# Kernel tuning notes

Hardware: AMD Instinct MI355X
Metric: run time of the kernel (lower is better)

Reference implementation:

```python
import jax, jax.numpy as jnp
import numpy as np
from jax import lax

B, S, D, H = 2, 2048, 1024, 16
DH = D // H
KERNELS = (3, 5)
NK = len(KERNELS)
COUT = D // NK  # channels per conv branch


def setup_inputs() -> dict:
    key = jax.random.key(0)
    ks = jax.random.split(key, 12)
    w = lambda k, shp: (jax.random.normal(k, shp, dtype=jnp.float32) * 0.02)
    inp = {
        "q": jax.random.normal(ks[0], (B, S, D), dtype=jnp.float32),
        "k": jax.random.normal(ks[1], (B, S, D), dtype=jnp.float32),
        "v": jax.random.normal(ks[2], (B, S, D), dtype=jnp.float32),
        "mask": jnp.ones((B, S, S), dtype=jnp.int32),
        "Wq": w(ks[3], (D, D)),
        "Wk": w(ks[4], (D, D)),
        "Wv": w(ks[5], (D, D)),
        "Wo": w(ks[6], (D, D)),
        "bo": jnp.zeros((D,), dtype=jnp.float32),
        "conv_w0": w(ks[7], (COUT, D, KERNELS[0])),  # OIH
        "conv_b0": jnp.zeros((COUT,), dtype=jnp.float32),
        "conv_w1": w(ks[8], (COUT, D, KERNELS[1])),
        "conv_b1": jnp.zeros((COUT,), dtype=jnp.float32),
        "gate": jnp.ones((H,), dtype=jnp.float32),
    }
    return inp


def _split_heads(x):  # [B,S,D] -> [B,H,S,DH]
    return x.reshape(B, S, H, DH).transpose(0, 2, 1, 3)


def _conv1d_same(x_ncl, w_oik, b, ksz):
    pad = ksz // 2
    y = lax.conv_general_dilated(
        x_ncl, w_oik, window_strides=(1,), padding=[(pad, pad)],
        dimension_numbers=("NCH", "OIH", "NCH"))
    return y + b[None, :, None]


def reference(q, k, v, mask, Wq, Wk, Wv, Wo, bo,
              conv_w0, conv_b0, conv_w1, conv_b1, gate):
    qh = _split_heads(q @ Wq.T)
    kh = _split_heads(k @ Wk.T)
    vh = _split_heads(v @ Wv.T)

    # conv-derived K: operate on raw k in NCL layout, concat channel-wise
    k_ncl = k.transpose(0, 2, 1)  # [B,D,S]
    c0 = _conv1d_same(k_ncl, conv_w0, conv_b0, KERNELS[0])
    c1 = _conv1d_same(k_ncl, conv_w1, conv_b1, KERNELS[1])
    k_conv = jnp.concatenate([c0, c1], axis=1).transpose(0, 2, 1)  # [B,S,D]
    kch = _split_heads(k_conv)

    g = jax.nn.sigmoid(gate).reshape(1, H, 1, 1)
    scale = 1.0 / np.sqrt(DH).astype(np.float32)
    attn = ((1.0 - g) * jnp.einsum("bhqd,bhkd->bhqk", qh, kh)
            + g * jnp.einsum("bhqd,bhkd->bhqk", qh, kch)) * scale
    attn = jnp.where(mask[:, None, :, :] == 0, jnp.float32(-1e9), attn)
    attn = jax.nn.softmax(attn, axis=-1)

    out = jnp.einsum("bhqk,bhkd->bhqd", attn, vh)  # [B,H,S,DH]
    out = out.transpose(0, 2, 1, 3).reshape(B, S, D)
    return out @ Wo.T + bo
```

## Files before the change

### kernel.cpp

```cpp
#include <hip/hip_runtime.h>
#include <math.h>

#define Bb 2
#define Ss 2048
#define Dd 1024
#define Hh 16
#define SP 2052

typedef unsigned short u16;
typedef __bf16 bf16x8 __attribute__((ext_vector_type(8)));
typedef float f32x4 __attribute__((ext_vector_type(4)));
typedef unsigned short u16x8 __attribute__((ext_vector_type(8)));

__device__ __forceinline__ u16 f2bf(float f) {
    union { float f; unsigned int u; } c; c.f = f;
    unsigned int u = c.u + 0x7FFFu + ((c.u >> 16) & 1u);
    return (u16)(u >> 16);
}

__device__ __forceinline__ float bf2f(u16 h) {
    union { unsigned int u; float f; } c; c.u = ((unsigned int)h) << 16;
    return c.f;
}

__device__ __forceinline__ void gload16(const void* g, void* l) {
    __builtin_amdgcn_global_load_lds(
        (const __attribute__((address_space(1))) void*)g,
        (__attribute__((address_space(3))) void*)l, 16, 0, 0);
}

__global__ void prep_weights(const float* __restrict__ Wq, const float* __restrict__ Wk,
                             const float* __restrict__ Wv, const float* __restrict__ Wo,
                             const float* __restrict__ w0, const float* __restrict__ b0,
                             const float* __restrict__ w1, const float* __restrict__ b1,
                             const float* __restrict__ gate,
                             u16* __restrict__ wqs, u16* __restrict__ wvb, u16* __restrict__ wob,
                             u16* __restrict__ Wc0, u16* __restrict__ Wc1, float* __restrict__ bc)
{
    int idx = blockIdx.x * 256 + threadIdx.x;
    const int NW = 1024 * 1024;
    if (idx < NW) { wqs[idx] = f2bf(Wq[idx] * 0.18033688011112042f); return; }
    idx -= NW;
    if (idx < NW) { wvb[idx] = f2bf(Wv[idx]); return; }
    idx -= NW;
    if (idx < NW) { wob[idx] = f2bf(Wo[idx]); return; }
    idx -= NW;
    if (idx < 512 * 3072) {
        int c = idx / 3072, rem = idx % 3072, t = rem >> 10, d = rem & 1023;
        float g = 1.f / (1.f + expf(-gate[c >> 6]));
        float v = g * w0[(c * 1024 + d) * 3 + t];
        if (t == 1) v += (1.f - g) * Wk[c * 1024 + d];
        Wc0[idx] = f2bf(v);
        return;
    }
    idx -= 512 * 3072;
    if (idx < 512 * 5120) {
        int c = idx / 5120, rem = idx % 5120, t = rem >> 10, d = rem & 1023;
        int cg = c + 512;
        float g = 1.f / (1.f + expf(-gate[cg >> 6]));
        float v = g * w1[(c * 1024 + d) * 5 + t];
        if (t == 2) v += (1.f - g) * Wk[cg * 1024 + d];
        Wc1[idx] = f2bf(v);
        return;
    }
    idx -= 512 * 5120;
    if (idx < 1024) {
        float g = 1.f / (1.f + expf(-gate[idx >> 6]));
        bc[idx] = g * (idx < 512 ? b0[idx] : b1[idx - 512]);
    }
}

__global__ void convert_inputs(const float* __restrict__ q, const float* __restrict__ k,
                               const float* __restrict__ v,
                               u16* __restrict__ qbf, u16* __restrict__ kbf, u16* __restrict__ vbf)
{
    int idx = blockIdx.x * 256 + threadIdx.x;
    const int per = (Bb * SP * Dd) / 8;
    int which = idx / per;
    if (which >= 3) return;
    int e = (idx - which * per) * 8;
    const float* src = which == 0 ? q : which == 1 ? k : v;
    u16* dst = which == 0 ? qbf : which == 1 ? kbf : vbf;
    int rp = e >> 10, col = e & 1023;
    int b = rp / SP, r = rp - b * SP;
    u16x8 o;
    if (r >= 2 && r < SP - 2) {
        const float* s = &src[((size_t)b * Ss + (r - 2)) * Dd + col];
        float4 lo = *(const float4*)s, hi = *(const float4*)(s + 4);
        o[0] = f2bf(lo.x); o[1] = f2bf(lo.y); o[2] = f2bf(lo.z); o[3] = f2bf(lo.w);
        o[4] = f2bf(hi.x); o[5] = f2bf(hi.y); o[6] = f2bf(hi.z); o[7] = f2bf(hi.w);
    } else {
        #pragma unroll
        for (int j = 0; j < 8; j++) o[j] = 0;
    }
    *(u16x8*)&dst[e] = o;
}

__global__ void mask_prep(const int* __restrict__ mask, unsigned int* __restrict__ bits,
                          int* __restrict__ rowflags)
{
    int row = blockIdx.x;
    int lane = threadIdx.x;
    const int* mp = mask + (size_t)row * Ss + lane * 32;
    unsigned int w = 0;
    #pragma unroll
    for (int j = 0; j < 32; j += 4) {
        int4 m4 = *(const int4*)&mp[j];
        if (m4.x != 0) w |= 1u << j;
        if (m4.y != 0) w |= 1u << (j + 1);
        if (m4.z != 0) w |= 1u << (j + 2);
        if (m4.w != 0) w |= 1u << (j + 3);
    }
    bits[(size_t)row * 64 + lane] = w;
    int anyz = __any(w != 0xFFFFFFFFu);
    if (lane == 0) rowflags[row] = anyz;
}

__device__ __forceinline__ void run_gemm_job(
    const u16* __restrict__ A, const u16* __restrict__ B, u16* __restrict__ C,
    int strB, int kS, int kL, int mB, int nB, int rO, int Cst,
    u16* As, u16* Bsh, int lane, int wave, int waveM, int waveN)
{
    f32x4 acc[4][4];
    #pragma unroll
    for (int i = 0; i < 4; i++)
        #pragma unroll
        for (int j = 0; j < 4; j++) acc[i][j] = (f32x4){0.f, 0.f, 0.f, 0.f};

    for (int k0 = kS; k0 < kS + kL; k0 += 32) {
        __syncthreads();
        #pragma unroll
        for (int cc = 0; cc < 2; cc++) {
            int rbase = (wave * 2 + cc) * 16;
            int r = rbase + (lane >> 2);
            int gm = mB + r;
            int grow = (gm >> 11) * SP + (gm & 2047) + rO + (k0 >> 10);
            int csrc = (lane & 3) ^ (r & 3);
            gload16(A + (size_t)grow * 1024 + (k0 & 1023) + csrc * 8, &As[rbase * 32]);
            int gn = nB + r;
            gload16(B + (size_t)gn * strB + k0 + csrc * 8, &Bsh[rbase * 32]);
        }
        __syncthreads();

        bf16x8 af[4], bfr[4];
        #pragma unroll
        for (int t = 0; t < 4; t++) {
            int mrow = waveM + t * 16 + (lane & 15);
            af[t] = *(const bf16x8*)&As[mrow * 32 + (((lane >> 4) ^ (mrow & 3))) * 8];
            int nrow = waveN + t * 16 + (lane & 15);
            bfr[t] = *(const bf16x8*)&Bsh[nrow * 32 + (((lane >> 4) ^ (nrow & 3))) * 8];
        }
        #pragma unroll
        for (int mt = 0; mt < 4; mt++)
            #pragma unroll
            for (int nt = 0; nt < 4; nt++)
                acc[mt][nt] = __builtin_amdgcn_mfma_f32_16x16x32_bf16(
                    af[mt], bfr[nt], acc[mt][nt], 0, 0, 0);
    }

    #pragma unroll
    for (int mt = 0; mt < 4; mt++)
        #pragma unroll
        for (int nt = 0; nt < 4; nt++)
            #pragma unroll
            for (int r = 0; r < 4; r++) {
                int row = mB + waveM + mt * 16 + (lane >> 4) * 4 + r;
                int gcol = nB + waveN + nt * 16 + (lane & 15);
                C[(size_t)row * Cst + gcol] = f2bf(acc[mt][nt][r]);
            }
}

__global__ __launch_bounds__(256) void gemm_multi(
    const u16* __restrict__ qbf, const u16* __restrict__ kbf, const u16* __restrict__ vbf,
    const u16* __restrict__ wqs, const u16* __restrict__ wvb,
    const u16* __restrict__ Wc0, const u16* __restrict__ Wc1,
    u16* __restrict__ Qp, u16* __restrict__ Vp,
    u16* __restrict__ P0a, u16* __restrict__ P0b,
    u16* __restrict__ P1a, u16* __restrict__ P1b, u16* __restrict__ P1c)
{
    __shared__ u16 As[128 * 32];
    __shared__ u16 Bsh[128 * 32];
    int tid = threadIdx.x, lane = tid & 63, wave = tid >> 6;
    int waveM = (wave >> 1) * 64, waveN = (wave & 1) * 64;

    int bid = blockIdx.x;
    const u16 *A0, *B0; u16 *C0; int sB0, kS0, kL0, mB0, nB0, rO0, Cs0;
    const u16 *A1 = nullptr, *B1 = nullptr; u16 *C1 = nullptr;
    int sB1 = 0, kS1 = 0, kL1 = 0, mB1 = 0, nB1 = 0, rO1 = 0, Cs1 = 0;
    int njobs = 1;

    if (bid < 128) {
        int t = bid;
        A0 = kbf; B0 = Wc0; C0 = P0a; sB0 = 3072; kS0 = 0; kL0 = 2048;
        mB0 = (t >> 2) * 128; nB0 = (t & 3) * 128; rO0 = 1; Cs0 = 512;
    } else if (bid < 256) {
        int t = bid - 128;
        A0 = kbf; B0 = Wc1; C0 = P1a; sB0 = 5120; kS0 = 0; kL0 = 2048;
        mB0 = (t >> 2) * 128; nB0 = (t & 3) * 128; rO0 = 0; Cs0 = 512;
    } else if (bid < 384) {
        int t = bid - 256;
        A0 = kbf; B0 = Wc1; C0 = P1b; sB0 = 5120; kS0 = 2048; kL0 = 2048;
        mB0 = (t >> 2) * 128; nB0 = (t & 3) * 128; rO0 = 0; Cs0 = 512;
    } else if (bid < 512) {
        int t = bid - 384;
        A0 = kbf; B0 = Wc0; C0 = P0b; sB0 = 3072; kS0 = 2048; kL0 = 1024;
        mB0 = (t >> 2) * 128; nB0 = (t & 3) * 128; rO0 = 1; Cs0 = 512;
        A1 = kbf; B1 = Wc1; C1 = P1c; sB1 = 5120; kS1 = 4096; kL1 = 1024;
        mB1 = mB0; nB1 = nB0; rO1 = 0; Cs1 = 512;
        njobs = 2;
    } else {
        int i0 = (bid - 512) * 2, i1 = i0 + 1;
        if (i0 < 256) { A0 = qbf; B0 = wqs; C0 = Qp; }
        else { i0 -= 256; A0 = vbf; B0 = wvb; C0 = Vp; }
        sB0 = 1024; kS0 = 0; kL0 = 1024;
        mB0 = (i0 >> 3) * 128; nB0 = (i0 & 7) * 128; rO0 = 2; Cs0 = 1024;
        if (i1 < 256) { A1 = qbf; B1 = wqs; C1 = Qp; }
        else { i1 -= 256; A1 = vbf; B1 = wvb; C1 = Vp; }
        sB1 = 1024; kS1 = 0; kL1 = 1024;
        mB1 = (i1 >> 3) * 128; nB1 = (i1 & 7) * 128; rO1 = 2; Cs1 = 1024;
        njobs = 2;
    }

    run_gemm_job(A0, B0, C0, sB0, kS0, kL0, mB0, nB0, rO0, Cs0,
                 As, Bsh, lane, wave, waveM, waveN);
    if (njobs == 2)
        run_gemm_job(A1, B1, C1, sB1, kS1, kL1, mB1, nB1, rO1, Cs1,
                     As, Bsh, lane, wave, waveM, waveN);
}

__global__ __launch_bounds__(256) void conv_reduce(
    const u16* __restrict__ P0a, const u16* __restrict__ P0b,
    const u16* __restrict__ P1a, const u16* __restrict__ P1b, const u16* __restrict__ P1c,
    const float* __restrict__ bc, u16* __restrict__ Keff)
{
    int idx = blockIdx.x * 256 + threadIdx.x;
    int e = idx * 8;
    int r = e >> 9, c = e & 511;
    u16x8 a0 = *(const u16x8*)&P0a[e];
    u16x8 b0 = *(const u16x8*)&P0b[e];
    u16x8 a1 = *(const u16x8*)&P1a[e];
    u16x8 b1 = *(const u16x8*)&P1b[e];
    u16x8 c1 = *(const u16x8*)&P1c[e];
    float bias0[8], bias1[8];
    *(float4*)&bias0[0] = *(const float4*)&bc[c];
    *(float4*)&bias0[4] = *(const float4*)&bc[c + 4];
    *(float4*)&bias1[0] = *(const float4*)&bc[512 + c];
    *(float4*)&bias1[4] = *(const float4*)&bc[512 + c + 4];
    u16x8 o0, o1;
    #pragma unroll
    for (int j = 0; j < 8; j++) {
        o0[j] = f2bf(bf2f(a0[j]) + bf2f(b0[j]) + bias0[j]);
        o1[j] = f2bf(bf2f(a1[j]) + bf2f(b1[j]) + bf2f(c1[j]) + bias1[j]);
    }
    *(u16x8*)&Keff[(size_t)r * 1024 + c] = o0;
    *(u16x8*)&Keff[(size_t)r * 1024 + 512 + c] = o1;
}

__global__ __launch_bounds__(256) void gemm_out(
    const u16* __restrict__ A, const u16* __restrict__ Bw,
    float* __restrict__ Cf32, const float* __restrict__ bias)
{
    __shared__ u16 As[128 * 32];
    __shared__ u16 Bs[128 * 32];
    int tid = threadIdx.x, lane = tid & 63, wave = tid >> 6;
    int waveM = (wave >> 1) * 64, waveN = (wave & 1) * 64;
    int mBase = blockIdx.y * 128, nBase = blockIdx.x * 128;
    const int K = 1024;

    f32x4 acc[4][4];
    #pragma unroll
    for (int i = 0; i < 4; i++)
        #pragma unroll
        for (int j = 0; j < 4; j++) acc[i][j] = (f32x4){0.f, 0.f, 0.f, 0.f};

    for (int k0 = 0; k0 < K; k0 += 32) {
        __syncthreads();
        #pragma unroll
        for (int cc = 0; cc < 2; cc++) {
            int rbase = (wave * 2 + cc) * 16;
            int r = rbase + (lane >> 2);
            int gm = mBase + r;
            int grow = (gm >> 11) * SP + (gm & 2047) + 2;
            int csrc = (lane & 3) ^ (r & 3);
            gload16(A + (size_t)grow * 1024 + k0 + csrc * 8, &As[rbase * 32]);
            int gn = nBase + r;
            gload16(Bw + (size_t)gn * K + k0 + csrc * 8, &Bs[rbase * 32]);
        }
        __syncthreads();

        bf16x8 af[4], bfr[4];
        #pragma unroll
        for (int t = 0; t < 4; t++) {
            int mrow = waveM + t * 16 + (lane & 15);
            af[t] = *(const bf16x8*)&As[mrow * 32 + (((lane >> 4) ^ (mrow & 3))) * 8];
            int nrow = waveN + t * 16 + (lane & 15);
            bfr[t] = *(const bf16x8*)&Bs[nrow * 32 + (((lane >> 4) ^ (nrow & 3))) * 8];
        }
        #pragma unroll
        for (int mt = 0; mt < 4; mt++)
            #pragma unroll
            for (int nt = 0; nt < 4; nt++)
                acc[mt][nt] = __builtin_amdgcn_mfma_f32_16x16x32_bf16(
                    af[mt], bfr[nt], acc[mt][nt], 0, 0, 0);
    }

    #pragma unroll
    for (int mt = 0; mt < 4; mt++)
        #pragma unroll
        for (int nt = 0; nt < 4; nt++)
            #pragma unroll
            for (int r = 0; r < 4; r++) {
                int row = mBase + waveM + mt * 16 + (lane >> 4) * 4 + r;
                int gcol = nBase + waveN + nt * 16 + (lane & 15);
                Cf32[(size_t)row * 1024 + gcol] = acc[mt][nt][r] + bias[gcol];
            }
}

__global__ __launch_bounds__(256) void vtrans_kernel(const u16* __restrict__ Vp,
                                                     u16* __restrict__ Vt)
{
    __shared__ u16 t[64 * 64];
    int bid = blockIdx.x;
    int st = bid & 31, h = (bid >> 5) & 15, b = bid >> 9;
    int s0 = st * 64;
    int tid = threadIdx.x;
    #pragma unroll
    for (int w = 0; w < 2; w++) {
        int f = tid + w * 256;
        int row = f >> 3, c = f & 7;
        int p = c ^ (row & 7);
        u16x8 v = *(const u16x8*)&Vp[(size_t)(b * Ss + s0 + row) * Dd + h * 64 + c * 8];
        *(u16x8*)&t[row * 64 + p * 8] = v;
    }
    __syncthreads();
    #pragma unroll
    for (int w = 0; w < 2; w++) {
        int f = tid + w * 256;
        int d = f >> 3, s8 = (f & 7) * 8;
        u16x8 v;
        #pragma unroll
        for (int j = 0; j < 8; j++) {
            int s = s8 + j;
            v[j] = t[s * 64 + (((d >> 3) ^ (s & 7))) * 8 + (d & 7)];
        }
        *(u16x8*)&Vt[((size_t)(b * Hh + h) * 64 + d) * Ss + s0 + s8] = v;
    }
}

__global__ __launch_bounds__(256) void flash_kernel(
    const u16* __restrict__ Qp, const u16* __restrict__ Keff, const u16* __restrict__ Vt,
    const unsigned int* __restrict__ maskbits, const int* __restrict__ rowflags,
    u16* __restrict__ AO)
{
    __shared__ u16 Qs[128 * 64];
    __shared__ u16 Ks[64 * 64];
    __shared__ u16 Ps[4][32 * 64];
    int tid = threadIdx.x, lane = tid & 63, wave = tid >> 6;
    int q0 = blockIdx.x * 128, h = blockIdx.y, b = blockIdx.z;

    #pragma unroll
    for (int cc = 0; cc < 4; cc++) {
        int rbase = (wave * 4 + cc) * 8;
        int r = rbase + (lane >> 3);
        int csrc = (lane & 7) ^ (r & 7);
        gload16(Qp + (size_t)(b * Ss + q0 + r) * Dd + h * 64 + csrc * 8, &Qs[rbase * 64]);
    }

    int anyz = 0;
    #pragma unroll
    for (int mt = 0; mt < 2; mt++)
        #pragma unroll
        for (int r = 0; r < 4; r++)
            anyz |= rowflags[b * Ss + q0 + wave * 32 + mt * 16 + (lane >> 4) * 4 + r];
    bool doMask = __any(anyz);

    float lrow[2][4];
    f32x4 oa[2][4];
    #pragma unroll
    for (int mt = 0; mt < 2; mt++) {
        #pragma unroll
        for (int r = 0; r < 4; r++) lrow[mt][r] = 0.f;
        #pragma unroll
        for (int nt = 0; nt < 4; nt++) oa[mt][nt] = (f32x4){0.f, 0.f, 0.f, 0.f};
    }

    __syncthreads();

    bf16x8 qa[2][2];
    #pragma unroll
    for (int mt = 0; mt < 2; mt++)
        #pragma unroll
        for (int ks = 0; ks < 2; ks++) {
            int mr = wave * 32 + mt * 16 + (lane & 15);
            int c = ks * 4 + (lane >> 4);
            qa[mt][ks] = *(const bf16x8*)&Qs[mr * 64 + (c ^ (mr & 7)) * 8];
        }

    const u16* vbase = Vt + (size_t)(b * Hh + h) * 64 * Ss;

    for (int k0 = 0; k0 < Ss; k0 += 64) {
        #pragma unroll
        for (int cc = 0; cc < 2; cc++) {
            int rbase = (wave * 2 + cc) * 8;
            int r = rbase + (lane >> 3);
            int csrc = (lane & 7) ^ (r & 7);
            gload16(Keff + (size_t)(b * Ss + k0 + r) * Dd + h * 64 + csrc * 8, &Ks[rbase * 64]);
        }
        __syncthreads();

        f32x4 sa[2][4];
        #pragma unroll
        for (int mt = 0; mt < 2; mt++)
            #pragma unroll
            for (int nt = 0; nt < 4; nt++) sa[mt][nt] = (f32x4){0.f, 0.f, 0.f, 0.f};
        bf16x8 kb[4][2];
        #pragma unroll
        for (int nt = 0; nt < 4; nt++)
            #pragma unroll
            for (int ks = 0; ks < 2; ks++) {
                int nr = nt * 16 + (lane & 15);
                int c = ks * 4 + (lane >> 4);
                kb[nt][ks] = *(const bf16x8*)&Ks[nr * 64 + (c ^ (nr & 7)) * 8];
            }
        #pragma unroll
        for (int mt = 0; mt < 2; mt++)
            #pragma unroll
            for (int nt = 0; nt < 4; nt++)
                #pragma unroll
                for (int ks = 0; ks < 2; ks++)
                    sa[mt][nt] = __builtin_amdgcn_mfma_f32_16x16x32_bf16(
                        qa[mt][ks], kb[nt][ks], sa[mt][nt], 0, 0, 0);

        bf16x8 vf[4][2];
        #pragma unroll
        for (int nt = 0; nt < 4; nt++)
            #pragma unroll
            for (int ks = 0; ks < 2; ks++) {
                int d = nt * 16 + (lane & 15);
                int kc = k0 + ks * 32 + (lane >> 4) * 8;
                vf[nt][ks] = *(const bf16x8*)&vbase[(size_t)d * Ss + kc];
            }

        if (doMask) {
            #pragma unroll
            for (int mt = 0; mt < 2; mt++)
                #pragma unroll
                for (int r = 0; r < 4; r++) {
                    int qrow = q0 + wave * 32 + mt * 16 + (lane >> 4) * 4 + r;
                    const unsigned int* mb = &maskbits[((size_t)b * Ss + qrow) * 64 + (k0 >> 5)];
                    unsigned int w0m = mb[0], w1m = mb[1];
                    #pragma unroll
                    for (int nt = 0; nt < 4; nt++) {
                        int col = nt * 16 + (lane & 15);
                        unsigned int w = (col & 32) ? w1m : w0m;
                        if (!((w >> (col & 31)) & 1u)) sa[mt][nt][r] = -1.442695e9f;
                    }
                }
        }

        #pragma unroll
        for (int mt = 0; mt < 2; mt++)
            #pragma unroll
            for (int r = 0; r < 4; r++) {
                float p0 = __builtin_amdgcn_exp2f(sa[mt][0][r]);
                float p1 = __builtin_amdgcn_exp2f(sa[mt][1][r]);
                float p2 = __builtin_amdgcn_exp2f(sa[mt][2][r]);
                float p3 = __builtin_amdgcn_exp2f(sa[mt][3][r]);
                sa[mt][0][r] = p0; sa[mt][1][r] = p1;
                sa[mt][2][r] = p2; sa[mt][3][r] = p3;
                lrow[mt][r] += (p0 + p1) + (p2 + p3);
            }

        u16* pw = Ps[wave];
        #pragma unroll
        for (int mt = 0; mt < 2; mt++)
            #pragma unroll
            for (int nt = 0; nt < 4; nt++)
                #pragma unroll
                for (int r = 0; r < 4; r++) {
                    int row = mt * 16 + (lane >> 4) * 4 + r;
                    int col = nt * 16 + (lane & 15);
                    pw[row * 64 + (((col >> 3) ^ (row & 7))) * 8 + (col & 7)] =
                        f2bf(sa[mt][nt][r]);
                }

        bf16x8 pa[2][2];
        #pragma unroll
        for (int mt = 0; mt < 2; mt++)
            #pragma unroll
            for (int ks = 0; ks < 2; ks++) {
                int row = mt * 16 + (lane & 15);
                int c = ks * 4 + (lane >> 4);
                pa[mt][ks] = *(const bf16x8*)&pw[row * 64 + (c ^ (row & 7)) * 8];
            }
        #pragma unroll
        for (int mt = 0; mt < 2; mt++)
            #pragma unroll
            for (int nt = 0; nt < 4; nt++)
                #pragma unroll
                for (int ks = 0; ks < 2; ks++)
                    oa[mt][nt] = __builtin_amdgcn_mfma_f32_16x16x32_bf16(
                        pa[mt][ks], vf[nt][ks], oa[mt][nt], 0, 0, 0);

        __syncthreads();
    }

    #pragma unroll
    for (int mt = 0; mt < 2; mt++)
        #pragma unroll
        for (int r = 0; r < 4; r++) {
            float rs = lrow[mt][r];
            #pragma unroll
            for (int d = 1; d < 16; d <<= 1) rs += __shfl_xor(rs, d, 64);
            float inv = 1.f / rs;
            int qrow = q0 + wave * 32 + mt * 16 + (lane >> 4) * 4 + r;
            size_t rowbase = ((size_t)b * SP + 2 + qrow) * Dd + h * 64;
            #pragma unroll
            for (int nt = 0; nt < 4; nt++)
                AO[rowbase + nt * 16 + (lane & 15)] = f2bf(oa[mt][nt][r] * inv);
        }
}

extern "C" void kernel_launch(void* const* d_in, const int* in_sizes, int n_in,
                              void* d_out, int out_size, void* d_ws, size_t ws_size,
                              hipStream_t stream)
{
    (void)in_sizes; (void)n_in; (void)out_size; (void)ws_size;
    const float* q    = (const float*)d_in[0];
    const float* k    = (const float*)d_in[1];
    const float* v    = (const float*)d_in[2];
    const int*   mask = (const int*)d_in[3];
    const float* Wq   = (const float*)d_in[4];
    const float* Wk   = (const float*)d_in[5];
    const float* Wv   = (const float*)d_in[6];
    const float* Wo   = (const float*)d_in[7];
    const float* bo   = (const float*)d_in[8];
    const float* w0   = (const float*)d_in[9];
    const float* b0   = (const float*)d_in[10];
    const float* w1   = (const float*)d_in[11];
    const float* b1   = (const float*)d_in[12];
    const float* gate = (const float*)d_in[13];
    float* out = (float*)d_out;

    char* p = (char*)d_ws;
    const size_t nPad = (size_t)Bb * SP * Dd;
    const size_t nBSD = (size_t)Bb * Ss * Dd;
    const size_t nHalf = (size_t)4096 * 512;
    u16* qbf  = (u16*)p;            p += nPad * 2;
    u16* kbf  = (u16*)p;            p += nPad * 2;
    u16* vbf  = (u16*)p;            p += nPad * 2;
    u16* Qp   = (u16*)p;            p += nBSD * 2;
    u16* Keff = (u16*)p;            p += nBSD * 2;
    u16* Vp   = (u16*)p;            p += nBSD * 2;
    u16* Vt   = (u16*)p;            p += nBSD * 2;
    u16* wqs  = (u16*)p;            p += (size_t)Dd * Dd * 2;
    u16* wvb  = (u16*)p;            p += (size_t)Dd * Dd * 2;
    u16* wob  = (u16*)p;            p += (size_t)Dd * Dd * 2;
    u16* Wc0  = (u16*)p;            p += (size_t)512 * 3072 * 2;
    u16* Wc1  = (u16*)p;            p += (size_t)512 * 5120 * 2;
    float* bc = (float*)p;          p += 1024 * 4;
    unsigned int* mbits = (unsigned int*)p; p += (size_t)Bb * Ss * 64 * 4;
    int* rflags = (int*)p;          p += (size_t)Bb * Ss * 4;
    u16* P1a = (u16*)p;             p += nHalf * 2;
    u16* P1b = (u16*)p;             p += nHalf * 2;
    u16* P1c = (u16*)p;             p += nHalf * 2;
    u16* P0a = Vt;
    u16* P0b = Vt + nHalf;
    u16* AO = vbf;

    {
        int total = 3 * 1024 * 1024 + 512 * 3072 + 512 * 5120 + 1024;
        hipLaunchKernelGGL(prep_weights, dim3((total + 255) / 256), dim3(256), 0, stream,
                           Wq, Wk, Wv, Wo, w0, b0, w1, b1, gate,
                           wqs, wvb, wob, Wc0, Wc1, bc);
    }
    {
        int total = 3 * (Bb * SP * Dd) / 8;
        hipLaunchKernelGGL(convert_inputs, dim3((total + 255) / 256), dim3(256), 0, stream,
                           q, k, v, qbf, kbf, vbf);
    }
    hipLaunchKernelGGL(mask_prep, dim3(Bb * Ss), dim3(64), 0, stream, mask, mbits, rflags);

    hipLaunchKernelGGL(gemm_multi, dim3(768), dim3(256), 0, stream,
                       qbf, kbf, vbf, wqs, wvb, Wc0, Wc1, Qp, Vp,
                       P0a, P0b, P1a, P1b, P1c);
    hipLaunchKernelGGL(conv_reduce, dim3(1024), dim3(256), 0, stream,
                       P0a, P0b, P1a, P1b, P1c, bc, Keff);
    hipLaunchKernelGGL(vtrans_kernel, dim3(Bb * Hh * (Ss / 64)), dim3(256), 0, stream, Vp, Vt);
    hipLaunchKernelGGL(flash_kernel, dim3(Ss / 128, Hh, Bb), dim3(256), 0, stream,
                       Qp, Keff, Vt, mbits, rflags, AO);
    hipLaunchKernelGGL(gemm_out, dim3(8, 32), dim3(256), 0, stream,
                       AO, wob, out, bo);
}
```

Baseline: 365.8 us.

## Double-buffer K tiles in flash loop, add MFMA priority, use native bf16 convert

The flash attention loop now keeps two LDS buffers for K. It prefetches the next K tile with global_load_lds while the current tile is being computed, which removes the barrier that used to sit right after each K load. V fragment loads are issued before the QK MFMAs so their latency is hidden. s_setprio is raised around the MFMA blocks, and the manual float-to-bf16 rounding is replaced with the compiler's native conversion. The cost is extra LDS for the second K buffer, which may lower occupancy. Correctness depends on the end-of-loop barrier also waiting on the outstanding async LDS loads.

```diff
diff --git a/kernel.cpp b/kernel.cpp
--- a/kernel.cpp
+++ b/kernel.cpp
@@ -16,6 +16,12 @@
     union { float f; unsigned int u; } c; c.f = f;
     unsigned int u = c.u + 0x7FFFu + ((c.u >> 16) & 1u);
     return (u16)(u >> 16);
+}
+
+__device__ __forceinline__ u16 f2bfn(float f) {
+    __bf16 h = (__bf16)f;
+    union { __bf16 h; u16 u; } c; c.h = h;
+    return c.u;
 }
 
 __device__ __forceinline__ float bf2f(u16 h) {
@@ -353,7 +359,7 @@
     u16* __restrict__ AO)
 {
     __shared__ u16 Qs[128 * 64];
-    __shared__ u16 Ks[64 * 64];
+    __shared__ u16 Ks[2][64 * 64];
     __shared__ u16 Ps[4][32 * 64];
     int tid = threadIdx.x, lane = tid & 63, wave = tid >> 6;
     int q0 = blockIdx.x * 128, h = blockIdx.y, b = blockIdx.z;
@@ -365,6 +371,13 @@
         int csrc = (lane & 7) ^ (r & 7);
         gload16(Qp + (size_t)(b * Ss + q0 + r) * Dd + h * 64 + csrc * 8, &Qs[rbase * 64]);
     }
+    #pragma unroll
+    for (int cc = 0; cc < 2; cc++) {
+        int rbase = (wave * 2 + cc) * 8;
+        int r = rbase + (lane >> 3);
+        int csrc = (lane & 7) ^ (r & 7);
+        gload16(Keff + (size_t)(b * Ss + r) * Dd + h * 64 + csrc * 8, &Ks[0][rbase * 64]);
+    }
 
     int anyz = 0;
     #pragma unroll
@@ -397,16 +410,34 @@
         }
 
     const u16* vbase = Vt + (size_t)(b * Hh + h) * 64 * Ss;
-
-    for (int k0 = 0; k0 < Ss; k0 += 64) {
-        #pragma unroll
-        for (int cc = 0; cc < 2; cc++) {
-            int rbase = (wave * 2 + cc) * 8;
-            int r = rbase + (lane >> 3);
-            int csrc = (lane & 7) ^ (r & 7);
-            gload16(Keff + (size_t)(b * Ss + k0 + r) * Dd + h * 64 + csrc * 8, &Ks[rbase * 64]);
-        }
-        __syncthreads();
+    const int NT = Ss / 64;
+
+    for (int t = 0; t < NT; t++) {
+        int k0 = t * 64;
+        const u16* kcur = Ks[t & 1];
+        u16* knxt = (u16*)Ks[(t + 1) & 1];
+
+        bf16x8 vf[4][2];
+        #pragma unroll
+        for (int nt = 0; nt < 4; nt++)
+            #pragma unroll
+            for (int ks = 0; ks < 2; ks++) {
+                int d = nt * 16 + (lane & 15);
+                int kc = k0 + ks * 32 + (lane >> 4) * 8;
+                vf[nt][ks] = *(const bf16x8*)&vbase[(size_t)d * Ss + kc];
+            }
+
+        if (t + 1 < NT) {
+            int kn = k0 + 64;
+            #pragma unroll
+            for (int cc = 0; cc < 2; cc++) {
+                int rbase = (wave * 2 + cc) * 8;
+                int r = rbase + (lane >> 3);
+                int csrc = (lane & 7) ^ (r & 7);
+                gload16(Keff + (size_t)(b * Ss + kn + r) * Dd + h * 64 + csrc * 8,
+                        &knxt[rbase * 64]);
+            }
+        }
 
         f32x4 sa[2][4];
         #pragma unroll
@@ -420,8 +451,9 @@
             for (int ks = 0; ks < 2; ks++) {
                 int nr = nt * 16 + (lane & 15);
                 int c = ks * 4 + (lane >> 4);
-                kb[nt][ks] = *(const bf16x8*)&Ks[nr * 64 + (c ^ (nr & 7)) * 8];
+                kb[nt][ks] = *(const bf16x8*)&kcur[nr * 64 + (c ^ (nr & 7)) * 8];
             }
+        __builtin_amdgcn_s_setprio(1);
         #pragma unroll
         for (int mt = 0; mt < 2; mt++)
             #pragma unroll
@@ -430,16 +462,7 @@
                 for (int ks = 0; ks < 2; ks++)
                     sa[mt][nt] = __builtin_amdgcn_mfma_f32_16x16x32_bf16(
                         qa[mt][ks], kb[nt][ks], sa[mt][nt], 0, 0, 0);
-
-        bf16x8 vf[4][2];
-        #pragma unroll
-        for (int nt = 0; nt < 4; nt++)
-            #pragma unroll
-            for (int ks = 0; ks < 2; ks++) {
-                int d = nt * 16 + (lane & 15);
-                int kc = k0 + ks * 32 + (lane >> 4) * 8;
-                vf[nt][ks] = *(const bf16x8*)&vbase[(size_t)d * Ss + kc];
-            }
+        __builtin_amdgcn_s_setprio(0);
 
         if (doMask) {
             #pragma unroll
@@ -481,7 +504,7 @@
                     int row = mt * 16 + (lane >> 4) * 4 + r;
                     int col = nt * 16 + (lane & 15);
                     pw[row * 64 + (((col >> 3) ^ (row & 7))) * 8 + (col & 7)] =
-                        f2bf(sa[mt][nt][r]);
+                        f2bfn(sa[mt][nt][r]);
                 }
 
         bf16x8 pa[2][2];
@@ -493,6 +516,7 @@
                 int c = ks * 4 + (lane >> 4);
                 pa[mt][ks] = *(const bf16x8*)&pw[row * 64 + (c ^ (row & 7)) * 8];
             }
+        __builtin_amdgcn_s_setprio(1);
         #pragma unroll
         for (int mt = 0; mt < 2; mt++)
             #pragma unroll
@@ -501,6 +525,7 @@
                 for (int ks = 0; ks < 2; ks++)
                     oa[mt][nt] = __builtin_amdgcn_mfma_f32_16x16x32_bf16(
                         pa[mt][ks], vf[nt][ks], oa[mt][nt], 0, 0, 0);
+        __builtin_amdgcn_s_setprio(0);
 
         __syncthreads();
     }
@@ -517,7 +542,7 @@
             size_t rowbase = ((size_t)b * SP + 2 + qrow) * Dd + h * 64;
             #pragma unroll
             for (int nt = 0; nt < 4; nt++)
-                AO[rowbase + nt * 16 + (lane & 15)] = f2bf(oa[mt][nt][r] * inv);
+                AO[rowbase + nt * 16 + (lane & 15)] = f2bfn(oa[mt][nt][r] * inv);
         }
 }
 
```

After: 426.3 us. +16.5%, slower.
